# Kernel optimization log

Measured on AMD Instinct MI355X. Metric: run time of the kernel, lower is better.

The kernel has to match this reference:

```python
import jax, jax.numpy as jnp
import numpy as np

B, C, Co, T, V, S, R, G = 64, 128, 128, 256, 25, 3, 16, 32
EPS = 1e-5


def setup_inputs() -> dict:
    key = jax.random.key(0)
    ks = jax.random.split(key, 12)
    sc = lambda fan: (2.0 / fan) ** 0.5  # kaiming fan_out-ish scale
    x = jax.random.normal(ks[0], (B, C, T, V), dtype=jnp.float32)
    Wq = jax.random.normal(ks[1], (S, R, C), dtype=jnp.float32) * sc(R)
    bq = jnp.zeros((S, R), dtype=jnp.float32)
    Wk = jax.random.normal(ks[2], (S, R, C), dtype=jnp.float32) * sc(R)
    bk = jnp.zeros((S, R), dtype=jnp.float32)
    Wv = jax.random.normal(ks[3], (S, Co, C), dtype=jnp.float32) * sc(Co)
    bv = jnp.zeros((S, Co), dtype=jnp.float32)
    Wr = jax.random.normal(ks[4], (S, Co, R), dtype=jnp.float32) * sc(Co)
    br = jnp.zeros((S, Co), dtype=jnp.float32)
    A = (jax.random.uniform(ks[5], (S, V, V), dtype=jnp.float32) < 0.15).astype(jnp.float32)
    alpha = jnp.zeros((1,), dtype=jnp.float32) + 0.1  # nonzero so relation path matters
    gn_w = jnp.full((Co,), 1e-6, dtype=jnp.float32)
    gn_b = jnp.zeros((Co,), dtype=jnp.float32)
    return {"x": x, "Wq": Wq, "bq": bq, "Wk": Wk, "bk": bk, "Wv": Wv, "bv": bv,
            "Wr": Wr, "br": br, "A": A, "alpha": alpha, "gn_w": gn_w, "gn_b": gn_b}


def reference(x, Wq, bq, Wk, bk, Wv, bv, Wr, br, A, alpha, gn_w, gn_b):
    # x: [B,C,T,V]. Mean over T commutes with the 1x1 conv (linear+bias).
    xm = x.mean(axis=2)                                          # [B,C,V]
    q = jnp.einsum('bcv,src->bsrv', xm, Wq) + bq[None, :, :, None]
    k = jnp.einsum('bcv,src->bsrv', xm, Wk) + bk[None, :, :, None]
    v = jnp.einsum('bctv,soc->bsotv', x, Wv) + bv[None, :, :, None, None]  # [B,S,Co,T,V]
    rel = jnp.tanh(q[..., :, None] - k[..., None, :])            # [B,S,R,V,V]
    relc = jnp.einsum('bsruv,sor->bsouv', rel, Wr) + br[None, :, :, None, None]
    relc = relc * alpha[0] + A[None, :, None, :, :]              # [B,S,Co,V,V]
    out = jnp.einsum('bsouv,bsotv->botu', relc, v)               # sum over subsets fused
    # GroupNorm(G, Co)
    o = out.reshape(B, G, Co // G, T, V)
    mu = o.mean(axis=(2, 3, 4), keepdims=True)
    var = ((o - mu) ** 2).mean(axis=(2, 3, 4), keepdims=True)
    o = ((o - mu) * jax.lax.rsqrt(var + EPS)).reshape(B, Co, T, V)
    o = o * gn_w[None, :, None, None] + gn_b[None, :, None, None]
    return jax.nn.relu(o + x)  # in==out -> identity residual
```

## Files before the change

kernel.cpp:

```cpp
#include <hip/hip_runtime.h>

#define BB 64
#define CC 128
#define CO 128
#define TTOT 256
#define VV 25
#define SS 3
#define RR 16
#define GG 32
#define EPSV 1e-5f

typedef __attribute__((ext_vector_type(8))) __bf16 bf16x8;
typedef __attribute__((ext_vector_type(4))) float f32x4;

static __device__ __forceinline__ ushort f2bf(float f) {
    unsigned u = __float_as_uint(f);
    u = (u + 0x7FFF + ((u >> 16) & 1)) >> 16;
    return (ushort)u;
}
static __device__ __forceinline__ ushort f2bf_fast(float f) {
    return (ushort)((__float_as_uint(f) + 0x8000u) >> 16);
}
static __device__ __forceinline__ float bf2f(ushort h) {
    return __uint_as_float(((unsigned)h) << 16);
}
static __device__ __forceinline__ f32x4 mfma16(bf16x8 a, bf16x8 b, f32x4 c) {
    return __builtin_amdgcn_mfma_f32_16x16x32_bf16(a, b, c, 0, 0, 0);
}

template<bool XB>
__global__ __launch_bounds__(256) void k_xmean(const float* __restrict__ x,
                                               float* __restrict__ xm,
                                               ushort* __restrict__ xb16) {
    int bc = blockIdx.x;
    const float* xp = x + (size_t)bc * (TTOT * VV);
    int t = threadIdx.x;
    float a[VV];
    const float* row = xp + t * VV;
#pragma unroll
    for (int v = 0; v < VV; ++v) a[v] = row[v];
    if (XB) {
        ushort* orow = xb16 + (size_t)bc * (TTOT * VV) + t * VV;
#pragma unroll
        for (int v = 0; v < VV; ++v) orow[v] = f2bf(a[v]);
    }
#pragma unroll
    for (int v = 0; v < VV; ++v) {
#pragma unroll
        for (int off = 32; off > 0; off >>= 1) a[v] += __shfl_down(a[v], off, 64);
    }
    __shared__ float sm[4][VV];
    int wave = t >> 6, lane = t & 63;
    if (lane == 0) {
#pragma unroll
        for (int v = 0; v < VV; ++v) sm[wave][v] = a[v];
    }
    __syncthreads();
    if (t < VV) {
        float s = sm[0][t] + sm[1][t] + sm[2][t] + sm[3][t];
        xm[(size_t)bc * VV + t] = s * (1.0f / TTOT);
    }
}

__global__ __launch_bounds__(512) void k_pack_wv(const float* __restrict__ Wv,
                                                 ushort* __restrict__ wvp) {
    int t = blockIdx.x * 512 + threadIdx.x;
    int lane = t & 63;
    int ks = (t >> 6) & 3;
    int mt = (t >> 8) & 1;
    int ob = (t >> 9) & 3;
    int s  = t >> 11;
    int o  = ob * 32 + mt * 16 + (lane & 15);
    int c0 = (ks * 4 + (lane >> 4)) * 8;
    const float* src = Wv + ((size_t)s * CO + o) * CC + c0;
    float4 a = *(const float4*)src;
    float4 b = *(const float4*)(src + 4);
    union { ushort us[8]; int4 v; } u;
    u.us[0] = f2bf(a.x); u.us[1] = f2bf(a.y); u.us[2] = f2bf(a.z); u.us[3] = f2bf(a.w);
    u.us[4] = f2bf(b.x); u.us[5] = f2bf(b.y); u.us[6] = f2bf(b.z); u.us[7] = f2bf(b.w);
    *(int4*)&wvp[(size_t)t * 8] = u.v;
}

__global__ __launch_bounds__(512) void k_qk(const float* __restrict__ xm,
    const float* __restrict__ Wq, const float* __restrict__ bq,
    const float* __restrict__ Wk, const float* __restrict__ bk,
    float* __restrict__ qb, float* __restrict__ kbuf) {
    int bs = blockIdx.x;
    int b = bs / SS, s = bs % SS;
    int tid = threadIdx.x;
    __shared__ float sxm[CC * VV];
    for (int i = tid; i < CC * VV; i += 512) sxm[i] = xm[(size_t)b * CC * VV + i];
    __syncthreads();
    if (tid < RR * VV) {
        int r = tid / VV, u = tid % VV;
        const float* wq = Wq + ((size_t)s * RR + r) * CC;
        const float* wk = Wk + ((size_t)s * RR + r) * CC;
        float aq = bq[s * RR + r], ak = bk[s * RR + r];
        for (int c = 0; c < CC; ++c) { float xv = sxm[c * VV + u]; aq += wq[c] * xv; ak += wk[c] * xv; }
        qb[bs * 400 + tid] = aq;
        kbuf[bs * 400 + tid] = ak;
    }
}

__global__ __launch_bounds__(256) void k_relcpack(const float* __restrict__ qb,
    const float* __restrict__ kbuf, const float* __restrict__ Wr,
    const float* __restrict__ br, const float* __restrict__ A,
    const float* __restrict__ alpha, ushort* __restrict__ rp) {
    int blk = blockIdx.x;
    int oc = blk & 7, bs = blk >> 3;
    int s = bs % SS;
    int tid = threadIdx.x;
    __shared__ float sq[RR * VV], sk[RR * VV];
    __shared__ float srel[RR][VV * VV];
    __shared__ ushort spack[16 * 1024];
    for (int i = tid; i < RR * VV; i += 256) { sq[i] = qb[bs * 400 + i]; sk[i] = kbuf[bs * 400 + i]; }
    __syncthreads();
    for (int i = tid; i < RR * VV * VV; i += 256) {
        int r = i / (VV * VV), uv = i % (VV * VV);
        srel[r][uv] = tanhf(sq[r * VV + uv / VV] - sk[r * VV + uv % VV]);
    }
    __syncthreads();
    float al = alpha[0];
    for (int i = tid; i < 512; i += 256) {
        int ol = i >> 5, u = i & 31;
        int o = oc * 16 + ol;
        ushort* dst = &spack[ol * 1024 + (u >> 4) * 512 + (u & 15) * 8];
        if (u < VV) {
            float acc[VV];
            float base = br[s * CO + o];
#pragma unroll
            for (int k = 0; k < VV; ++k) acc[k] = base;
            const float* wr = Wr + ((size_t)s * CO + o) * RR;
#pragma unroll
            for (int r = 0; r < RR; ++r) {
                float w = wr[r];
                const float* sr = &srel[r][u * VV];
#pragma unroll
                for (int k = 0; k < VV; ++k) acc[k] += w * sr[k];
            }
            const float* Ab = A + (size_t)s * VV * VV + u * VV;
#pragma unroll
            for (int kb4 = 0; kb4 < 4; ++kb4) {
                union { ushort us[8]; int4 v; } pk;
#pragma unroll
                for (int j = 0; j < 8; ++j) {
                    int kk = kb4 * 8 + j;
                    pk.us[j] = (kk < VV) ? f2bf(acc[kk] * al + Ab[kk]) : (ushort)0;
                }
                *(int4*)&dst[kb4 * 128] = pk.v;
            }
        } else {
#pragma unroll
            for (int kb4 = 0; kb4 < 4; ++kb4)
                *(int4*)&dst[kb4 * 128] = int4{0, 0, 0, 0};
        }
    }
    __syncthreads();
    int4* dstg = (int4*)(rp + ((size_t)bs * CO + oc * 16) * 1024);
    const int4* srcs = (const int4*)spack;
    for (int i = tid; i < 2048; i += 256) dstg[i] = srcs[i];
}

template<bool XB>
__global__ __launch_bounds__(512, 4) void k_main(const void* __restrict__ xsrc,
    const ushort* __restrict__ wvp, const float* __restrict__ bv,
    const ushort* __restrict__ rp, ushort* __restrict__ outw,
    float* __restrict__ stats) {
    int bid = blockIdx.x;
    int b = (bid & 7) + 8 * (bid >> 8);
    int tch = (bid >> 3) & 31;
    int tid = threadIdx.x;
    int wvi = tid >> 6;
    int lane = tid & 63;
    int g4 = lane >> 4, l15 = lane & 15;
    int mt = wvi & 1, sb = wvi >> 1;

    __shared__ ushort s_xt[16 * 1600];
    __shared__ ushort s_v[32 * 256];
    __shared__ float s_bv[SS * CO];

    if (tid < SS * CO) s_bv[tid] = bv[tid];
    if (tid < 256) {
        int o = tid >> 3, t = tid & 7;
        *(int4*)&s_v[o * 256 + 192 + t * 8] = int4{0, 0, 0, 0};
    }

    const ushort* rpb = rp + (size_t)b * (SS * CO * 1024) + wvi * 4096 + g4 * 128 + l15 * 8;
    const ushort* wpb = wvp + mt * 2048 + lane * 8;

    bf16x8 af[4], bf[4][2];
#pragma unroll
    for (int ks = 0; ks < 4; ++ks) af[ks] = *(const bf16x8*)&wpb[ks * 512];
#pragma unroll
    for (int oi = 0; oi < 4; ++oi) {
        bf[oi][0] = *(const bf16x8*)&rpb[oi * 1024];
        bf[oi][1] = *(const bf16x8*)&rpb[oi * 1024 + 512];
    }

    if (XB) {
        const ushort* xb = (const ushort*)xsrc + (size_t)b * (CC * TTOT * VV) + tch * 200;
        for (int id = wvi; id < 64; id += 8) {
            int c8 = id >> 2, seg = id & 3;
            int n = seg * 64 + lane;
            if (n < 200) {
                union { ushort us[8]; int4 v4; } u;
#pragma unroll
                for (int cc = 0; cc < 8; ++cc)
                    u.us[cc] = xb[(size_t)(c8 * 8 + cc) * (TTOT * VV) + n];
                *(int4*)&s_xt[c8 * 1600 + n * 8] = u.v4;
            }
        }
    } else {
        const float* xb = (const float*)xsrc + (size_t)b * (CC * TTOT * VV) + tch * 200;
        for (int id = wvi; id < 64; id += 8) {
            int c8 = id >> 2, seg = id & 3;
            int n = seg * 64 + lane;
            if (n < 200) {
                union { ushort us[8]; int4 v4; } u;
#pragma unroll
                for (int cc = 0; cc < 8; ++cc)
                    u.us[cc] = f2bf(xb[(size_t)(c8 * 8 + cc) * (TTOT * VV) + n]);
                *(int4*)&s_xt[c8 * 1600 + n * 8] = u.v4;
            }
        }
    }

    int xo[4], vbx[4];
    bool sv[4];
#pragma unroll
    for (int i = 0; i < 4; ++i) {
        int nt = sb + 4 * i;
        int n = nt * 16 + l15;
        bool valid = (n < 200);
        sv[i] = valid;
        int nn = valid ? n : 0;
        xo[i] = nn * 8;
        int t = nn / 25, k = nn % 25;
        vbx[i] = ((k >> 3) * 64 + t * 8 + (k & 7)) ^ (g4 << 3);
    }
    int avoff[4];
#pragma unroll
    for (int oi = 0; oi < 4; ++oi)
        avoff[oi] = (wvi * 4 + oi) * 256 + g4 * 64 + (((l15 & 7) * 8) ^ ((wvi & 3) << 3));

    f32x4 acc2[4][2];
#pragma unroll
    for (int oi = 0; oi < 4; ++oi) { acc2[oi][0] = f32x4{0,0,0,0}; acc2[oi][1] = f32x4{0,0,0,0}; }
    float psum[4], pqsum[4];

#pragma unroll
    for (int st = 0; st < 12; ++st) {
        const int ob = st / 3, ss = st % 3;
        __syncthreads();
        float4 bvv = *(const float4*)&s_bv[ss * CO + ob * 32 + mt * 16 + g4 * 4];

#pragma unroll
        for (int i = 0; i < 4; ++i) {
            f32x4 d = f32x4{0,0,0,0};
#pragma unroll
            for (int ks = 0; ks < 4; ++ks)
                d = mfma16(af[ks], *(const bf16x8*)&s_xt[(ks * 4 + g4) * 1600 + xo[i]], d);
            if (sv[i]) {
                int rowb = mt * 16 + g4 * 4;
                s_v[(rowb    ) * 256 + vbx[i]] = f2bf_fast(d[0] + bvv.x);
                s_v[(rowb + 1) * 256 + vbx[i]] = f2bf_fast(d[1] + bvv.y);
                s_v[(rowb + 2) * 256 + vbx[i]] = f2bf_fast(d[2] + bvv.z);
                s_v[(rowb + 3) * 256 + vbx[i]] = f2bf_fast(d[3] + bvv.w);
            }
        }
        if (st < 11) {
            const ushort* w1 = wpb + (((st + 1) % 3) * 4 + (st + 1) / 3) * 4096;
#pragma unroll
            for (int ks = 0; ks < 4; ++ks) af[ks] = *(const bf16x8*)&w1[ks * 512];
        }
        __syncthreads();

#pragma unroll
        for (int oi = 0; oi < 4; ++oi) {
            bf16x8 av = *(const bf16x8*)&s_v[avoff[oi]];
            acc2[oi][0] = mfma16(av, bf[oi][0], acc2[oi][0]);
            acc2[oi][1] = mfma16(av, bf[oi][1], acc2[oi][1]);
        }
        if (st < 11) {
            const ushort* r1 = rpb + ((st + 1) % 3) * 131072 + ((st + 1) / 3) * 32768;
#pragma unroll
            for (int oi = 0; oi < 4; ++oi) {
                bf[oi][0] = *(const bf16x8*)&r1[oi * 1024];
                bf[oi][1] = *(const bf16x8*)&r1[oi * 1024 + 512];
            }
        }

        if (ss == 2) {
            float ps = 0.f, pq = 0.f;
#pragma unroll
            for (int oi = 0; oi < 4; ++oi) {
                int o = ob * 32 + wvi * 4 + oi;
                if (g4 < 2) {
                    size_t obase = (((size_t)b * CO + o) * TTOT + tch * 8 + g4 * 4) * VV;
#pragma unroll
                    for (int ut = 0; ut < 2; ++ut) {
                        int u = ut * 16 + l15;
                        if (u < VV) {
#pragma unroll
                            for (int r = 0; r < 4; ++r) {
                                float val = acc2[oi][ut][r];
                                outw[obase + (size_t)r * VV + u] = f2bf_fast(val);
                                ps += val; pq += val * val;
                            }
                        }
                    }
                }
                acc2[oi][0] = f32x4{0,0,0,0};
                acc2[oi][1] = f32x4{0,0,0,0};
            }
            psum[ob] = ps; pqsum[ob] = pq;
        }
    }

#pragma unroll
    for (int ob = 0; ob < 4; ++ob) {
        float ps = psum[ob], pq = pqsum[ob];
#pragma unroll
        for (int off = 16; off > 0; off >>= 1) {
            ps += __shfl_down(ps, off, 64);
            pq += __shfl_down(pq, off, 64);
        }
        if (lane == 0) {
            atomicAdd(&stats[b * (GG * 2) + (ob * 8 + wvi) * 2], ps);
            atomicAdd(&stats[b * (GG * 2) + (ob * 8 + wvi) * 2 + 1], pq);
        }
    }
}

template<bool XB>
__global__ __launch_bounds__(256) void k_final(float* __restrict__ out,
    const ushort* __restrict__ outw, const void* __restrict__ xsrc,
    const float* __restrict__ stats,
    const float* __restrict__ gw, const float* __restrict__ gb) {
    size_t i = ((size_t)blockIdx.x * 256 + threadIdx.x) * 4;
    int o = (int)((i / (TTOT * VV)) % CO);
    int b = (int)(i / ((size_t)CO * TTOT * VV));
    int gg = o >> 2;
    float s0 = stats[b * (GG * 2) + gg * 2];
    float s1 = stats[b * (GG * 2) + gg * 2 + 1];
    const float inv = 1.0f / (4 * TTOT * VV);
    float mu = s0 * inv;
    float var = s1 * inv - mu * mu;
    float rs = rsqrtf(var + EPSV) * gw[o];
    float sh = gb[o] - mu * rs;

    ushort4 rw = *(const ushort4*)(outw + i);
    float4 xr;
    if (XB) {
        ushort4 xw = *(const ushort4*)((const ushort*)xsrc + i);
        xr.x = bf2f(xw.x); xr.y = bf2f(xw.y); xr.z = bf2f(xw.z); xr.w = bf2f(xw.w);
    } else {
        xr = *(const float4*)((const float*)xsrc + i);
    }
    float4 res;
    res.x = fmaxf(bf2f(rw.x) * rs + sh + xr.x, 0.f);
    res.y = fmaxf(bf2f(rw.y) * rs + sh + xr.y, 0.f);
    res.z = fmaxf(bf2f(rw.z) * rs + sh + xr.z, 0.f);
    res.w = fmaxf(bf2f(rw.w) * rs + sh + xr.w, 0.f);
    *(float4*)(out + i) = res;
}

extern "C" void kernel_launch(void* const* d_in, const int* in_sizes, int n_in,
                              void* d_out, int out_size, void* d_ws, size_t ws_size,
                              hipStream_t stream) {
    const float* x     = (const float*)d_in[0];
    const float* Wq    = (const float*)d_in[1];
    const float* bq    = (const float*)d_in[2];
    const float* Wk    = (const float*)d_in[3];
    const float* bk    = (const float*)d_in[4];
    const float* Wv    = (const float*)d_in[5];
    const float* bv    = (const float*)d_in[6];
    const float* Wr    = (const float*)d_in[7];
    const float* br    = (const float*)d_in[8];
    const float* A     = (const float*)d_in[9];
    const float* alpha = (const float*)d_in[10];
    const float* gw    = (const float*)d_in[11];
    const float* gb    = (const float*)d_in[12];
    float* out = (float*)d_out;

    float*  xm    = (float*)d_ws;
    float*  stats = xm + (size_t)BB * CC * VV;
    ushort* wvp   = (ushort*)(stats + (size_t)BB * GG * 2);
    ushort* rp    = wvp + 49152;
    ushort* outw  = rp + (size_t)BB * SS * CO * 1024;
    ushort* xb16  = outw + (size_t)BB * CO * TTOT * VV;
    float*  qb    = (float*)outw;
    float*  kbuf  = qb + (size_t)BB * SS * RR * VV;

    size_t need_fixed = 819200 + 16384 + 98304 + 50331648 + 104857600;
    size_t need_xb = need_fixed + 104857600;
    bool xbp = (ws_size >= need_xb);

    hipMemsetAsync(stats, 0, (size_t)BB * GG * 2 * sizeof(float), stream);
    if (xbp) k_xmean<true><<<BB * CC, 256, 0, stream>>>(x, xm, xb16);
    else     k_xmean<false><<<BB * CC, 256, 0, stream>>>(x, xm, xb16);
    k_pack_wv<<<12, 512, 0, stream>>>(Wv, wvp);
    k_qk<<<BB * SS, 512, 0, stream>>>(xm, Wq, bq, Wk, bk, qb, kbuf);
    k_relcpack<<<BB * SS * 8, 256, 0, stream>>>(qb, kbuf, Wr, br, A, alpha, rp);
    int nfin = (BB * CO * TTOT * VV) / (256 * 4);
    if (xbp) {
        k_main<true><<<2048, 512, 0, stream>>>(xb16, wvp, bv, rp, outw, stats);
        k_final<true><<<nfin, 256, 0, stream>>>(out, outw, xb16, stats, gw, gb);
    } else {
        k_main<false><<<2048, 512, 0, stream>>>(x, wvp, bv, rp, outw, stats);
        k_final<false><<<nfin, 256, 0, stream>>>(out, outw, x, stats, gw, gb);
    }
}
```

Measured before the change: 465.5 us.

## Pre-transpose x into channel-packed padded bf16 layout and fold value bias into relation matrix

Replaces the mean kernel with a transpose kernel that writes x as 8-channel-packed bf16 with V padded to 32, and computes the T-mean in the same pass. The main kernel then loads its tile with contiguous 16-byte loads instead of strided per-channel gathers. It also restructures the MFMA work split: each wave computes 32 output rows over 32 columns. The value bias is folded into an extra relation column paired with a constant-one row, which removes the per-element bias add. The residual now reads fp32 x directly, and the padded layout adds some memory traffic plus an extra sync per stage.

```diff
diff --git a/kernel.cpp b/kernel.cpp
--- a/kernel.cpp
+++ b/kernel.cpp
@@ -28,38 +28,40 @@
     return __builtin_amdgcn_mfma_f32_16x16x32_bf16(a, b, c, 0, 0, 0);
 }
 
-template<bool XB>
-__global__ __launch_bounds__(256) void k_xmean(const float* __restrict__ x,
-                                               float* __restrict__ xm,
-                                               ushort* __restrict__ xb16) {
-    int bc = blockIdx.x;
-    const float* xp = x + (size_t)bc * (TTOT * VV);
-    int t = threadIdx.x;
-    float a[VV];
-    const float* row = xp + t * VV;
-#pragma unroll
-    for (int v = 0; v < VV; ++v) a[v] = row[v];
-    if (XB) {
-        ushort* orow = xb16 + (size_t)bc * (TTOT * VV) + t * VV;
-#pragma unroll
-        for (int v = 0; v < VV; ++v) orow[v] = f2bf(a[v]);
-    }
-#pragma unroll
-    for (int v = 0; v < VV; ++v) {
-#pragma unroll
-        for (int off = 32; off > 0; off >>= 1) a[v] += __shfl_down(a[v], off, 64);
-    }
-    __shared__ float sm[4][VV];
-    int wave = t >> 6, lane = t & 63;
-    if (lane == 0) {
-#pragma unroll
-        for (int v = 0; v < VV; ++v) sm[wave][v] = a[v];
-    }
-    __syncthreads();
-    if (t < VV) {
-        float s = sm[0][t] + sm[1][t] + sm[2][t] + sm[3][t];
-        xm[(size_t)bc * VV + t] = s * (1.0f / TTOT);
-    }
+__global__ __launch_bounds__(512) void k_xpose(const float* __restrict__ x,
+                                               ushort* __restrict__ xg,
+                                               float* __restrict__ xm) {
+    int bid = blockIdx.x;
+    int b = bid >> 4, c8 = bid & 15;
+    int tid = threadIdx.x;
+    __shared__ float sx[8 * 800];
+    float xsum = 0.f;
+    const float* xb = x + ((size_t)b * CC + c8 * 8) * (TTOT * VV);
+    ushort* xo = xg + (size_t)bid * 8192 * 8;
+    int cc = tid / VV, vv = tid % VV;
+    for (int ti = 0; ti < 8; ++ti) {
+        for (int i = tid; i < 1600; i += 512) {
+            int c = i / 200, q = i % 200;
+            *(float4*)&sx[c * 800 + q * 4] =
+                *(const float4*)&xb[(size_t)c * (TTOT * VV) + ti * 800 + q * 4];
+        }
+        __syncthreads();
+        for (int i = tid; i < 1024; i += 512) {
+            int t = i >> 5, k = i & 31;
+            union { ushort us[8]; int4 v4; } u;
+            if (k < VV) {
+#pragma unroll
+                for (int c = 0; c < 8; ++c) u.us[c] = f2bf(sx[c * 800 + t * VV + k]);
+            } else u.v4 = int4{0, 0, 0, 0};
+            *(int4*)&xo[(size_t)((ti * 32 + t) * 32 + k) * 8] = u.v4;
+        }
+        if (tid < 200) {
+#pragma unroll
+            for (int t = 0; t < 32; ++t) xsum += sx[cc * 800 + t * VV + vv];
+        }
+        __syncthreads();
+    }
+    if (tid < 200) xm[((size_t)b * CC + c8 * 8 + cc) * VV + vv] = xsum * (1.0f / TTOT);
 }
 
 __global__ __launch_bounds__(512) void k_pack_wv(const float* __restrict__ Wv,
@@ -105,7 +107,8 @@
 __global__ __launch_bounds__(256) void k_relcpack(const float* __restrict__ qb,
     const float* __restrict__ kbuf, const float* __restrict__ Wr,
     const float* __restrict__ br, const float* __restrict__ A,
-    const float* __restrict__ alpha, ushort* __restrict__ rp) {
+    const float* __restrict__ alpha, const float* __restrict__ bv,
+    ushort* __restrict__ rp) {
     int blk = blockIdx.x;
     int oc = blk & 7, bs = blk >> 3;
     int s = bs % SS;
@@ -139,13 +142,18 @@
                 for (int k = 0; k < VV; ++k) acc[k] += w * sr[k];
             }
             const float* Ab = A + (size_t)s * VV * VV + u * VV;
+            float vals[VV]; float rsum = 0.f;
+#pragma unroll
+            for (int k = 0; k < VV; ++k) { vals[k] = acc[k] * al + Ab[k]; rsum += vals[k]; }
+            float bvt = bv[s * CO + o] * rsum;
 #pragma unroll
             for (int kb4 = 0; kb4 < 4; ++kb4) {
                 union { ushort us[8]; int4 v; } pk;
 #pragma unroll
                 for (int j = 0; j < 8; ++j) {
                     int kk = kb4 * 8 + j;
-                    pk.us[j] = (kk < VV) ? f2bf(acc[kk] * al + Ab[kk]) : (ushort)0;
+                    pk.us[j] = (kk < VV) ? f2bf(vals[kk])
+                             : (kk == VV) ? f2bf(bvt) : (ushort)0;
                 }
                 *(int4*)&dst[kb4 * 128] = pk.v;
             }
@@ -161,132 +169,113 @@
     for (int i = tid; i < 2048; i += 256) dstg[i] = srcs[i];
 }
 
-template<bool XB>
-__global__ __launch_bounds__(512, 4) void k_main(const void* __restrict__ xsrc,
-    const ushort* __restrict__ wvp, const float* __restrict__ bv,
-    const ushort* __restrict__ rp, ushort* __restrict__ outw,
-    float* __restrict__ stats) {
+__global__ __launch_bounds__(512, 4) void k_main(const ushort* __restrict__ xg,
+    const ushort* __restrict__ wvp, const ushort* __restrict__ rp,
+    ushort* __restrict__ outw, float* __restrict__ stats) {
     int bid = blockIdx.x;
     int b = (bid & 7) + 8 * (bid >> 8);
     int tch = (bid >> 3) & 31;
     int tid = threadIdx.x;
-    int wvi = tid >> 6;
-    int lane = tid & 63;
-    int g4 = lane >> 4, l15 = lane & 15;
-    int mt = wvi & 1, sb = wvi >> 1;
-
-    __shared__ ushort s_xt[16 * 1600];
+    int wvi = tid >> 6, lane = tid & 63, g4 = lane >> 4, l15 = lane & 15;
+
+    __shared__ ushort s_xt[16 * 2048];
     __shared__ ushort s_v[32 * 256];
-    __shared__ float s_bv[SS * CO];
-
-    if (tid < SS * CO) s_bv[tid] = bv[tid];
-    if (tid < 256) {
-        int o = tid >> 3, t = tid & 7;
-        *(int4*)&s_v[o * 256 + 192 + t * 8] = int4{0, 0, 0, 0};
-    }
-
-    const ushort* rpb = rp + (size_t)b * (SS * CO * 1024) + wvi * 4096 + g4 * 128 + l15 * 8;
-    const ushort* wpb = wvp + mt * 2048 + lane * 8;
-
-    bf16x8 af[4], bf[4][2];
-#pragma unroll
-    for (int ks = 0; ks < 4; ++ks) af[ks] = *(const bf16x8*)&wpb[ks * 512];
+
+    if (tid < 256) s_v[(tid >> 3) * 256 + (tid & 7) * 32 + 25] = 0x3F80;
+
+    const ushort* wfb = wvp + lane * 8;
+    const ushort* rfb = rp + ((size_t)b * SS * CO + wvi * 4) * 1024 + g4 * 128 + l15 * 8;
+
+    bf16x8 af[2][4], bf[4][2];
+#pragma unroll
+    for (int m = 0; m < 2; ++m)
+#pragma unroll
+        for (int ks = 0; ks < 4; ++ks) af[m][ks] = *(const bf16x8*)&wfb[(m * 4 + ks) * 512];
 #pragma unroll
     for (int oi = 0; oi < 4; ++oi) {
-        bf[oi][0] = *(const bf16x8*)&rpb[oi * 1024];
-        bf[oi][1] = *(const bf16x8*)&rpb[oi * 1024 + 512];
-    }
-
-    if (XB) {
-        const ushort* xb = (const ushort*)xsrc + (size_t)b * (CC * TTOT * VV) + tch * 200;
-        for (int id = wvi; id < 64; id += 8) {
-            int c8 = id >> 2, seg = id & 3;
-            int n = seg * 64 + lane;
-            if (n < 200) {
-                union { ushort us[8]; int4 v4; } u;
-#pragma unroll
-                for (int cc = 0; cc < 8; ++cc)
-                    u.us[cc] = xb[(size_t)(c8 * 8 + cc) * (TTOT * VV) + n];
-                *(int4*)&s_xt[c8 * 1600 + n * 8] = u.v4;
-            }
-        }
-    } else {
-        const float* xb = (const float*)xsrc + (size_t)b * (CC * TTOT * VV) + tch * 200;
-        for (int id = wvi; id < 64; id += 8) {
-            int c8 = id >> 2, seg = id & 3;
-            int n = seg * 64 + lane;
-            if (n < 200) {
-                union { ushort us[8]; int4 v4; } u;
-#pragma unroll
-                for (int cc = 0; cc < 8; ++cc)
-                    u.us[cc] = f2bf(xb[(size_t)(c8 * 8 + cc) * (TTOT * VV) + n]);
-                *(int4*)&s_xt[c8 * 1600 + n * 8] = u.v4;
-            }
-        }
-    }
-
-    int xo[4], vbx[4];
-    bool sv[4];
-#pragma unroll
-    for (int i = 0; i < 4; ++i) {
-        int nt = sb + 4 * i;
-        int n = nt * 16 + l15;
-        bool valid = (n < 200);
-        sv[i] = valid;
-        int nn = valid ? n : 0;
-        xo[i] = nn * 8;
-        int t = nn / 25, k = nn % 25;
-        vbx[i] = ((k >> 3) * 64 + t * 8 + (k & 7)) ^ (g4 << 3);
-    }
-    int avoff[4];
-#pragma unroll
-    for (int oi = 0; oi < 4; ++oi)
-        avoff[oi] = (wvi * 4 + oi) * 256 + g4 * 64 + (((l15 & 7) * 8) ^ ((wvi & 3) << 3));
+        bf[oi][0] = *(const bf16x8*)&rfb[(size_t)oi * 1024];
+        bf[oi][1] = *(const bf16x8*)&rfb[(size_t)oi * 1024 + 512];
+    }
+
+    const ushort* xgb = xg + ((size_t)b * 16 * 8192 + (size_t)tch * 256) * 8;
+    for (int i = tid; i < 4096; i += 512) {
+        int c8 = i >> 8, nl = i & 255;
+        *(int4*)&s_xt[c8 * 2048 + nl * 8] = *(const int4*)&xgb[((size_t)c8 * 8192 + nl) * 8];
+    }
 
     f32x4 acc2[4][2];
 #pragma unroll
     for (int oi = 0; oi < 4; ++oi) { acc2[oi][0] = f32x4{0,0,0,0}; acc2[oi][1] = f32x4{0,0,0,0}; }
     float psum[4], pqsum[4];
 
-#pragma unroll
+    int nl0 = wvi * 32 + l15;
+    int nl1 = nl0 + 16;
+    bool wr1 = (l15 != 9);
+    int avo = (l15 & 7) * 32 + g4 * 8;
+
+    __syncthreads();
+
     for (int st = 0; st < 12; ++st) {
-        const int ob = st / 3, ss = st % 3;
+        int ob = st >> 2 == 0 ? 0 : 0;
+        ob = st / 3;
+        int ss = st - ob * 3;
+
+        {
+            f32x4 d0 = {0,0,0,0}, d1 = {0,0,0,0};
+#pragma unroll
+            for (int ks = 0; ks < 4; ++ks) {
+                bf16x8 bx = *(const bf16x8*)&s_xt[(ks * 4 + g4) * 2048 + nl0 * 8];
+                d0 = mfma16(af[0][ks], bx, d0);
+                d1 = mfma16(af[1][ks], bx, d1);
+            }
+#pragma unroll
+            for (int r = 0; r < 4; ++r) {
+                s_v[(g4 * 4 + r) * 256 + nl0]      = f2bf_fast(d0[r]);
+                s_v[(16 + g4 * 4 + r) * 256 + nl0] = f2bf_fast(d1[r]);
+            }
+        }
+        {
+            f32x4 d0 = {0,0,0,0}, d1 = {0,0,0,0};
+#pragma unroll
+            for (int ks = 0; ks < 4; ++ks) {
+                bf16x8 bx = *(const bf16x8*)&s_xt[(ks * 4 + g4) * 2048 + nl1 * 8];
+                d0 = mfma16(af[0][ks], bx, d0);
+                d1 = mfma16(af[1][ks], bx, d1);
+            }
+            if (wr1) {
+#pragma unroll
+                for (int r = 0; r < 4; ++r) {
+                    s_v[(g4 * 4 + r) * 256 + nl1]      = f2bf_fast(d0[r]);
+                    s_v[(16 + g4 * 4 + r) * 256 + nl1] = f2bf_fast(d1[r]);
+                }
+            }
+        }
         __syncthreads();
-        float4 bvv = *(const float4*)&s_bv[ss * CO + ob * 32 + mt * 16 + g4 * 4];
-
-#pragma unroll
-        for (int i = 0; i < 4; ++i) {
-            f32x4 d = f32x4{0,0,0,0};
-#pragma unroll
-            for (int ks = 0; ks < 4; ++ks)
-                d = mfma16(af[ks], *(const bf16x8*)&s_xt[(ks * 4 + g4) * 1600 + xo[i]], d);
-            if (sv[i]) {
-                int rowb = mt * 16 + g4 * 4;
-                s_v[(rowb    ) * 256 + vbx[i]] = f2bf_fast(d[0] + bvv.x);
-                s_v[(rowb + 1) * 256 + vbx[i]] = f2bf_fast(d[1] + bvv.y);
-                s_v[(rowb + 2) * 256 + vbx[i]] = f2bf_fast(d[2] + bvv.z);
-                s_v[(rowb + 3) * 256 + vbx[i]] = f2bf_fast(d[3] + bvv.w);
-            }
-        }
+
         if (st < 11) {
-            const ushort* w1 = wpb + (((st + 1) % 3) * 4 + (st + 1) / 3) * 4096;
-#pragma unroll
-            for (int ks = 0; ks < 4; ++ks) af[ks] = *(const bf16x8*)&w1[ks * 512];
-        }
-        __syncthreads();
+            int st1 = st + 1;
+            int ob1 = st1 / 3, ss1 = st1 - ob1 * 3;
+            const ushort* w1 = wfb + (ss1 * 4 + ob1) * 4096;
+#pragma unroll
+            for (int m = 0; m < 2; ++m)
+#pragma unroll
+                for (int ks = 0; ks < 4; ++ks) af[m][ks] = *(const bf16x8*)&w1[(m * 4 + ks) * 512];
+        }
 
 #pragma unroll
         for (int oi = 0; oi < 4; ++oi) {
-            bf16x8 av = *(const bf16x8*)&s_v[avoff[oi]];
+            bf16x8 av = *(const bf16x8*)&s_v[(wvi * 4 + oi) * 256 + avo];
             acc2[oi][0] = mfma16(av, bf[oi][0], acc2[oi][0]);
             acc2[oi][1] = mfma16(av, bf[oi][1], acc2[oi][1]);
         }
         if (st < 11) {
-            const ushort* r1 = rpb + ((st + 1) % 3) * 131072 + ((st + 1) / 3) * 32768;
+            int st1 = st + 1;
+            int ob1 = st1 / 3, ss1 = st1 - ob1 * 3;
+            const ushort* r1 = rfb + ((size_t)ss1 * CO + ob1 * 32) * 1024;
 #pragma unroll
             for (int oi = 0; oi < 4; ++oi) {
-                bf[oi][0] = *(const bf16x8*)&r1[oi * 1024];
-                bf[oi][1] = *(const bf16x8*)&r1[oi * 1024 + 512];
+                bf[oi][0] = *(const bf16x8*)&r1[(size_t)oi * 1024];
+                bf[oi][1] = *(const bf16x8*)&r1[(size_t)oi * 1024 + 512];
             }
         }
 
@@ -315,6 +304,7 @@
             }
             psum[ob] = ps; pqsum[ob] = pq;
         }
+        __syncthreads();
     }
 
 #pragma unroll
@@ -332,9 +322,8 @@
     }
 }
 
-template<bool XB>
 __global__ __launch_bounds__(256) void k_final(float* __restrict__ out,
-    const ushort* __restrict__ outw, const void* __restrict__ xsrc,
+    const ushort* __restrict__ outw, const float* __restrict__ x,
     const float* __restrict__ stats,
     const float* __restrict__ gw, const float* __restrict__ gb) {
     size_t i = ((size_t)blockIdx.x * 256 + threadIdx.x) * 4;
@@ -350,13 +339,7 @@
     float sh = gb[o] - mu * rs;
 
     ushort4 rw = *(const ushort4*)(outw + i);
-    float4 xr;
-    if (XB) {
-        ushort4 xw = *(const ushort4*)((const ushort*)xsrc + i);
-        xr.x = bf2f(xw.x); xr.y = bf2f(xw.y); xr.z = bf2f(xw.z); xr.w = bf2f(xw.w);
-    } else {
-        xr = *(const float4*)((const float*)xsrc + i);
-    }
+    float4 xr = *(const float4*)(x + i);
     float4 res;
     res.x = fmaxf(bf2f(rw.x) * rs + sh + xr.x, 0.f);
     res.y = fmaxf(bf2f(rw.y) * rs + sh + xr.y, 0.f);
@@ -388,26 +371,15 @@
     ushort* wvp   = (ushort*)(stats + (size_t)BB * GG * 2);
     ushort* rp    = wvp + 49152;
     ushort* outw  = rp + (size_t)BB * SS * CO * 1024;
-    ushort* xb16  = outw + (size_t)BB * CO * TTOT * VV;
+    ushort* xg    = outw + (size_t)BB * CO * TTOT * VV;
     float*  qb    = (float*)outw;
     float*  kbuf  = qb + (size_t)BB * SS * RR * VV;
 
-    size_t need_fixed = 819200 + 16384 + 98304 + 50331648 + 104857600;
-    size_t need_xb = need_fixed + 104857600;
-    bool xbp = (ws_size >= need_xb);
-
     hipMemsetAsync(stats, 0, (size_t)BB * GG * 2 * sizeof(float), stream);
-    if (xbp) k_xmean<true><<<BB * CC, 256, 0, stream>>>(x, xm, xb16);
-    else     k_xmean<false><<<BB * CC, 256, 0, stream>>>(x, xm, xb16);
+    k_xpose<<<BB * 16, 512, 0, stream>>>(x, xg, xm);
     k_pack_wv<<<12, 512, 0, stream>>>(Wv, wvp);
     k_qk<<<BB * SS, 512, 0, stream>>>(xm, Wq, bq, Wk, bk, qb, kbuf);
-    k_relcpack<<<BB * SS * 8, 256, 0, stream>>>(qb, kbuf, Wr, br, A, alpha, rp);
-    int nfin = (BB * CO * TTOT * VV) / (256 * 4);
-    if (xbp) {
-        k_main<true><<<2048, 512, 0, stream>>>(xb16, wvp, bv, rp, outw, stats);
-        k_final<true><<<nfin, 256, 0, stream>>>(out, outw, xb16, stats, gw, gb);
-    } else {
-        k_main<false><<<2048, 512, 0, stream>>>(x, wvp, bv, rp, outw, stats);
-        k_final<false><<<nfin, 256, 0, stream>>>(out, outw, x, stats, gw, gb);
-    }
-}
+    k_relcpack<<<BB * SS * 8, 256, 0, stream>>>(qb, kbuf, Wr, br, A, alpha, bv, rp);
+    k_main<<<2048, 512, 0, stream>>>(xg, wvp, rp, outw, stats);
+    k_final<<<(BB * CO * TTOT * VV) / (256 * 4), 256, 0, stream>>>(out, outw, x, stats, gw, gb);
+}
```

Result: slower. 510.4 us (+9.6%).
